# Performance work log

Measured on AMD Instinct MI355X. Metric: run time of the kernel, lower is better.

The kernel has to match this reference:

```python
import jax, jax.numpy as jnp
import numpy as np

D_MODEL = 1024
NUM_HEADS = 16
D_H = D_MODEL // NUM_HEADS
BATCH, SEQ = 4, 2048


def setup_inputs() -> dict:
    key = jax.random.key(0)
    kx, kq, kk, kv, ko = jax.random.split(key, 5)
    sigma = (2.0 / (D_MODEL + D_MODEL)) ** 0.5

    def trunc(k):
        return jax.random.truncated_normal(k, -3.0, 3.0, (D_MODEL, D_MODEL), dtype=jnp.float32) * sigma

    return {
        "x": jax.random.normal(kx, (BATCH, SEQ, D_MODEL), dtype=jnp.float32),
        "Wq": trunc(kq),
        "Wk": trunc(kk),
        "Wv": trunc(kv),
        "Wo": trunc(ko),
    }


def reference(x, Wq, Wk, Wv, Wo):
    B, S, D = x.shape
    H, Dh = NUM_HEADS, D_H
    # Linear: einsum('d_out d_in, ... d_in -> ... d_out')
    q = jnp.einsum('oi,bsi->bso', Wq, x)
    k = jnp.einsum('oi,bsi->bso', Wk, x)
    v = jnp.einsum('oi,bsi->bso', Wv, x)
    # split heads: [B, H, S, Dh]
    q = q.reshape(B, S, H, Dh).transpose(0, 2, 1, 3)
    k = k.reshape(B, S, H, Dh).transpose(0, 2, 1, 3)
    v = v.reshape(B, S, H, Dh).transpose(0, 2, 1, 3)
    scale = 1.0 / jnp.sqrt(jnp.asarray(Dh, dtype=x.dtype))
    score = jnp.einsum('bhnd,bhmd->bhnm', q, k) * scale  # [B,H,S,S]
    causal = jnp.tril(jnp.ones((S, S), dtype=bool))
    score = jnp.where(causal, score, -jnp.inf)
    attn = jax.nn.softmax(score, axis=-1)
    out = jnp.einsum('bhnm,bhmd->bhnd', attn, v)
    out = out.transpose(0, 2, 1, 3).reshape(B, S, D)
    return jnp.einsum('oi,bsi->bso', Wo, out)
```

## Files before the change

kernel.cpp:

```cpp
#include <hip/hip_runtime.h>
#include <hip/hip_bf16.h>

typedef __bf16 bf16x8 __attribute__((ext_vector_type(8)));
typedef __bf16 bf16x4 __attribute__((ext_vector_type(4)));
typedef float f32x4 __attribute__((ext_vector_type(4)));
typedef float f32x16 __attribute__((ext_vector_type(16)));

#define NB 4
#define NS 2048
#define ND 1024
#define NH 16
#define NDH 64
#define NM (NB*NS)

#define MFMA(a,b,c)   __builtin_amdgcn_mfma_f32_16x16x32_bf16((a),(b),(c),0,0,0)
#define MFMA32(a,b,c) __builtin_amdgcn_mfma_f32_32x32x16_bf16((a),(b),(c),0,0,0)

__device__ __forceinline__ void gload16(const void* g, void* l) {
    __builtin_amdgcn_global_load_lds(
        (const __attribute__((address_space(1))) void*)(g),
        (__attribute__((address_space(3))) void*)(l),
        16, 0, 0);
}

__device__ __forceinline__ unsigned cvt_pk_bf16(float lo, float hi) {
    unsigned w;
    asm("v_cvt_pk_bf16_f32 %0, %1, %2" : "=v"(w) : "v"(lo), "v"(hi));
    return w;
}
__device__ __forceinline__ float fmax3(float a, float b, float c) {
    float d;
    asm("v_max3_f32 %0, %1, %2, %3" : "=v"(d) : "v"(a), "v"(b), "v"(c));
    return d;
}
#define PLSWAP(a, b) asm("v_permlane32_swap_b32 %0, %1" : "+v"(a), "+v"(b))

__global__ __launch_bounds__(256) void cast4(const float* __restrict__ in,
                                             __bf16* __restrict__ out, int n) {
    int i = (blockIdx.x * 256 + threadIdx.x) * 4;
    if (i >= n) return;
    float4 v = *(const float4*)(in + i);
    bf16x4 o;
    o[0] = (__bf16)v.x; o[1] = (__bf16)v.y; o[2] = (__bf16)v.z; o[3] = (__bf16)v.w;
    *(bf16x4*)(out + i) = o;
}

__global__ __launch_bounds__(256) void cast4w(
    const float* __restrict__ w0, const float* __restrict__ w1,
    const float* __restrict__ w2, const float* __restrict__ w3,
    __bf16* __restrict__ o0, __bf16* __restrict__ o1,
    __bf16* __restrict__ o2, __bf16* __restrict__ o3) {
    const int z = blockIdx.y;
    const float* in  = (z == 0) ? w0 : (z == 1) ? w1 : (z == 2) ? w2 : w3;
    __bf16*      out = (z == 0) ? o0 : (z == 1) ? o1 : (z == 2) ? o2 : o3;
    int i = (blockIdx.x * 256 + threadIdx.x) * 4;
    float4 v = *(const float4*)(in + i);
    bf16x4 o;
    o[0] = (__bf16)v.x; o[1] = (__bf16)v.y; o[2] = (__bf16)v.z; o[3] = (__bf16)v.w;
    *(bf16x4*)(out + i) = o;
}

template<int MODE>
__global__ __launch_bounds__(256) void gemm128(
    const __bf16* __restrict__ A,
    const __bf16* __restrict__ W0, const __bf16* __restrict__ W1,
    const __bf16* __restrict__ W2,
    __bf16* __restrict__ O0, __bf16* __restrict__ O1, __bf16* __restrict__ O2,
    float* __restrict__ Cf)
{
    __shared__ alignas(16) __bf16 SB[2 * 128 * 32];
    __bf16* As = SB;
    __bf16* Bs = SB + 128 * 32;

    const int tid  = threadIdx.x;
    const int wave = tid >> 6, lane = tid & 63;
    const int l16  = lane & 15, lq = lane >> 4;
    const int bm = blockIdx.x * 128;
    const int bn = blockIdx.y * 128;
    const int z  = (MODE == 0) ? blockIdx.z : 0;
    const __bf16* __restrict__ Bw =
        (MODE == 0) ? ((z == 0) ? W0 : (z == 1) ? W1 : W2) : W0;

    const int wr = (wave >> 1) * 64;
    const int wc = (wave & 1) * 64;

    f32x4 acc[4][4];
    #pragma unroll
    for (int i = 0; i < 4; i++)
        #pragma unroll
        for (int j = 0; j < 4; j++)
            acc[i][j] = (f32x4){0.f, 0.f, 0.f, 0.f};

    const int ch0 = tid, ch1 = tid + 256;
    const int r0 = ch0 >> 2, c0 = (ch0 & 3) * 8;
    const int r1 = ch1 >> 2, c1 = (ch1 & 3) * 8;

    for (int k0 = 0; k0 < ND; k0 += 32) {
        __syncthreads();
        gload16(A  + (size_t)(bm + r0) * ND + k0 + c0, As + ch0 * 8);
        gload16(Bw + (size_t)(bn + r0) * ND + k0 + c0, Bs + ch0 * 8);
        gload16(A  + (size_t)(bm + r1) * ND + k0 + c1, As + ch1 * 8);
        gload16(Bw + (size_t)(bn + r1) * ND + k0 + c1, Bs + ch1 * 8);
        __syncthreads();

        bf16x8 af[4], bf[4];
        #pragma unroll
        for (int i = 0; i < 4; i++) {
            af[i] = *(const bf16x8*)(As + (wr + i*16 + l16) * 32 + lq * 8);
            bf[i] = *(const bf16x8*)(Bs + (wc + i*16 + l16) * 32 + lq * 8);
        }
        #pragma unroll
        for (int i = 0; i < 4; i++)
            #pragma unroll
            for (int j = 0; j < 4; j++)
                acc[i][j] = MFMA(af[i], bf[j], acc[i][j]);
    }

    if (MODE == 0 && z == 2) {
        __bf16* T = SB;
        const int TP = 136;
        #pragma unroll 1
        for (int c = 0; c < 4; ++c) {
            __syncthreads();
            #pragma unroll
            for (int j = 0; j < 4; j++) {
                if (((wc + j * 16) >> 5) != c) continue;
                #pragma unroll
                for (int i = 0; i < 4; i++)
                    #pragma unroll
                    for (int r = 0; r < 4; r++) {
                        int row = wr + i*16 + lq*4 + r;
                        int col = wc + j*16 + l16 - c*32;
                        T[col * TP + row] = (__bf16)acc[i][j][r];
                    }
            }
            __syncthreads();
            #pragma unroll
            for (int u2 = 0; u2 < 2; u2++) {
                int idx  = tid + u2 * 256;
                int trow = idx >> 4, tu = idx & 15;
                int gcol = bn + c*32 + trow;
                int gs   = bm + tu * 8;
                bf16x8 val = *(const bf16x8*)&T[trow * TP + tu * 8];
                int hh = gcol >> 6, dh = gcol & 63;
                *(bf16x8*)&O2[(((size_t)(gs >> 11) * NH + hh) * NDH + dh) * NS
                              + (gs & 2047)] = val;
            }
        }
        return;
    }

    #pragma unroll
    for (int i = 0; i < 4; i++) {
        #pragma unroll
        for (int j = 0; j < 4; j++) {
            #pragma unroll
            for (int r = 0; r < 4; r++) {
                int row = bm + wr + i*16 + lq*4 + r;
                int col = bn + wc + j*16 + l16;
                float v = acc[i][j][r];
                if (MODE == 1) {
                    Cf[(size_t)row * ND + col] = v;
                } else {
                    if (z == 0) v *= 0.1803368801111204f;
                    int b = row >> 11, s = row & 2047;
                    int h = col >> 6,  dh = col & 63;
                    __bf16* dst = (z == 0) ? O0 : O1;
                    dst[(((size_t)b*NH + h)*NS + s)*NDH + dh] = (__bf16)v;
                }
            }
        }
    }
}

__global__ __launch_bounds__(256) void attn_st(
    const __bf16* __restrict__ Q, const __bf16* __restrict__ K,
    const __bf16* __restrict__ Vt, __bf16* __restrict__ Oa)
{
    __shared__ alignas(16) __bf16 Ks[32*64];
    __shared__ alignas(16) __bf16 Vs[64*32];
    __shared__ float Fs[4][32];

    const int tid  = threadIdx.x;
    const int wave = tid >> 6, lane = tid & 63;
    const int qq   = lane & 31, hi = lane >> 5;

    const int bid = blockIdx.x;
    const int jg  = 15 - (bid >> 6);
    const int bh  = (bid & 7) * 8 + ((bid >> 3) & 7);
    const int j   = 4 * jg + wave;
    const int q0  = 32 * j;
    const int nt  = 4 * jg + 4;

    const int b = bh >> 4, h = bh & 15;
    const size_t qkb = (size_t)bh * NS * NDH;
    const size_t vbb = (size_t)bh * NDH * NS;
    float* Fw = Fs[wave];

    bf16x8 qf[4];
    {
        const __bf16* qr = Q + qkb + (size_t)(q0 + qq) * NDH + hi * 8;
        #pragma unroll
        for (int c = 0; c < 4; c++) qf[c] = *(const bf16x8*)(qr + c * 16);
    }

    f32x16 o0 = (f32x16)0.f, o1 = (f32x16)0.f;
    float mr = -__builtin_inff(), lsum = 0.f;

    const int kr = tid >> 3, ku = tid & 7;
    const int vd = tid >> 2, vu = tid & 3;
    const __bf16* ksrc = K  + qkb + (size_t)kr * NDH + (size_t)((ku ^ (kr & 7)) * 8);
    const __bf16* vsrc = Vt + vbb + (size_t)vd * NS  + (size_t)((vu ^ ((vd >> 1) & 3)) * 8);
    __bf16* kdst = Ks + tid * 8;
    __bf16* vdst = Vs + tid * 8;

    const int vsw = (qq >> 1) & 3;

    #pragma unroll 1
    for (int t = 0; t < nt; ++t) {
        __syncthreads();
        gload16(ksrc, kdst);
        gload16(vsrc, vdst);
        asm volatile("s_waitcnt vmcnt(0)" ::: "memory");
        __syncthreads();

        if (t <= j) {
            bf16x8 kf[4], vf[4];
            #pragma unroll
            for (int c = 0; c < 4; c++)
                kf[c] = *(const bf16x8*)(Ks + qq * 64 + ((2 * c + hi) ^ (qq & 7)) * 8);
            vf[0] = *(const bf16x8*)(Vs + qq * 32        + ((hi)     ^ vsw) * 8);
            vf[1] = *(const bf16x8*)(Vs + qq * 32        + ((2 + hi) ^ vsw) * 8);
            vf[2] = *(const bf16x8*)(Vs + (qq + 32) * 32 + ((hi)     ^ vsw) * 8);
            vf[3] = *(const bf16x8*)(Vs + (qq + 32) * 32 + ((2 + hi) ^ vsw) * 8);

            f32x16 s = (f32x16)0.f;
            __builtin_amdgcn_s_setprio(1);
            #pragma unroll
            for (int c = 0; c < 4; c++) s = MFMA32(kf[c], qf[c], s);
            __builtin_amdgcn_s_setprio(0);

            if (t == j) {
                #pragma unroll
                for (int r = 0; r < 16; r++) {
                    const int crow = (r & 3) + 8 * (r >> 2) + 4 * hi;
                    if (crow > qq) s[r] = -__builtin_inff();
                }
            }

            float a0 = fmax3(s[0],  s[1],  s[2]);
            float a1 = fmax3(s[3],  s[4],  s[5]);
            float a2 = fmax3(s[6],  s[7],  s[8]);
            float a3 = fmax3(s[9],  s[10], s[11]);
            float a4 = fmax3(s[12], s[13], s[14]);
            float tm = fmaxf(fmax3(a0, a1, a2), fmax3(a3, a4, s[15]));

            if (__any(tm > mr + 8.f)) {
                float rowm = fmaxf(tm, __shfl_xor(tm, 32));
                float mnew = fmaxf(mr, rowm);
                float fac  = exp2f(mr - mnew);
                mr = mnew; lsum *= fac;
                if (lane < 32) Fw[qq] = fac;
                f32x4 f0 = *(const f32x4*)&Fw[4 * hi];
                f32x4 f1 = *(const f32x4*)&Fw[8 + 4 * hi];
                f32x4 f2 = *(const f32x4*)&Fw[16 + 4 * hi];
                f32x4 f3 = *(const f32x4*)&Fw[24 + 4 * hi];
                #pragma unroll
                for (int i = 0; i < 4; i++) {
                    o0[i]      *= f0[i]; o1[i]      *= f0[i];
                    o0[4 + i]  *= f1[i]; o1[4 + i]  *= f1[i];
                    o0[8 + i]  *= f2[i]; o1[8 + i]  *= f2[i];
                    o0[12 + i] *= f3[i]; o1[12 + i] *= f3[i];
                }
            }

            float pv[16]; float psum = 0.f;
            #pragma unroll
            for (int r = 0; r < 16; r++) { pv[r] = exp2f(s[r] - mr); psum += pv[r]; }
            lsum += psum;

            unsigned w0 = cvt_pk_bf16(pv[0],  pv[1]);
            unsigned w1 = cvt_pk_bf16(pv[2],  pv[3]);
            unsigned w2 = cvt_pk_bf16(pv[4],  pv[5]);
            unsigned w3 = cvt_pk_bf16(pv[6],  pv[7]);
            unsigned w4 = cvt_pk_bf16(pv[8],  pv[9]);
            unsigned w5 = cvt_pk_bf16(pv[10], pv[11]);
            unsigned w6 = cvt_pk_bf16(pv[12], pv[13]);
            unsigned w7 = cvt_pk_bf16(pv[14], pv[15]);
            PLSWAP(w0, w2); PLSWAP(w1, w3);
            PLSWAP(w4, w6); PLSWAP(w5, w7);
            bf16x8 pa0 = __builtin_bit_cast(bf16x8, (uint4){w0, w1, w2, w3});
            bf16x8 pa1 = __builtin_bit_cast(bf16x8, (uint4){w4, w5, w6, w7});

            __builtin_amdgcn_s_setprio(1);
            o0 = MFMA32(pa0, vf[0], o0);
            o0 = MFMA32(pa1, vf[1], o0);
            o1 = MFMA32(pa0, vf[2], o1);
            o1 = MFMA32(pa1, vf[3], o1);
            __builtin_amdgcn_s_setprio(0);
        }

        ksrc += 32 * NDH;
        vsrc += 32;
    }

    lsum += __shfl_xor(lsum, 32);
    if (lane < 32) Fw[qq] = 1.f / lsum;
    f32x4 i0 = *(const f32x4*)&Fw[4 * hi];
    f32x4 i1 = *(const f32x4*)&Fw[8 + 4 * hi];
    f32x4 i2 = *(const f32x4*)&Fw[16 + 4 * hi];
    f32x4 i3 = *(const f32x4*)&Fw[24 + 4 * hi];
    __bf16* ob = Oa + ((size_t)b * NS + q0) * ND + h * 64 + qq;
    #pragma unroll
    for (int g2 = 0; g2 < 4; g2++) {
        f32x4 iv = (g2 == 0) ? i0 : (g2 == 1) ? i1 : (g2 == 2) ? i2 : i3;
        #pragma unroll
        for (int i = 0; i < 4; i++) {
            const int row = 8 * g2 + 4 * hi + i;
            ob[(size_t)row * ND]      = (__bf16)(o0[4 * g2 + i] * iv[i]);
            ob[(size_t)row * ND + 32] = (__bf16)(o1[4 * g2 + i] * iv[i]);
        }
    }
}

extern "C" void kernel_launch(void* const* d_in, const int* in_sizes, int n_in,
                              void* d_out, int out_size, void* d_ws, size_t ws_size,
                              hipStream_t stream) {
    const float* x  = (const float*)d_in[0];
    const float* wq = (const float*)d_in[1];
    const float* wk = (const float*)d_in[2];
    const float* wv = (const float*)d_in[3];
    const float* wo = (const float*)d_in[4];
    char* ws = (char*)d_ws;

    __bf16* xb  = (__bf16*)(ws);
    __bf16* wqb = (__bf16*)(ws + (16ull << 20));
    __bf16* wkb = (__bf16*)(ws + (18ull << 20));
    __bf16* wvb = (__bf16*)(ws + (20ull << 20));
    __bf16* wob = (__bf16*)(ws + (22ull << 20));
    __bf16* Qb  = (__bf16*)(ws + (24ull << 20));
    __bf16* Kb  = (__bf16*)(ws + (40ull << 20));
    __bf16* Vtb = (__bf16*)(ws + (56ull << 20));
    __bf16* Ab  = (__bf16*)(ws + (72ull << 20));
    float* out  = (float*)d_out;

    cast4<<<dim3(NM * ND / 1024), 256, 0, stream>>>(x, xb, NM * ND);
    cast4w<<<dim3(ND * ND / 1024, 4), 256, 0, stream>>>(
        wq, wk, wv, wo, wqb, wkb, wvb, wob);

    gemm128<0><<<dim3(NM/128, ND/128, 3), 256, 0, stream>>>(
        xb, wqb, wkb, wvb, Qb, Kb, Vtb, nullptr);

    attn_st<<<dim3(1024), 256, 0, stream>>>(Qb, Kb, Vtb, Ab);

    gemm128<1><<<dim3(NM/128, ND/128), 256, 0, stream>>>(
        Ab, wob, nullptr, nullptr, nullptr, nullptr, nullptr, out);
}
```

Baseline: 186.9 us.

## Fuse x cast into QKV GEMM, widen GEMM tiles, register-prefetch attention K/V

Drops the separate fp32-to-bf16 cast kernel for x. The QKV GEMM now loads fp32 x directly, converts it in registers and writes it to swizzled LDS, prefetching the next k-slice. The GEMMs move to 128x256 tiles with K=64 steps, 512 threads and an XOR swizzle to cut LDS bank conflicts. The attention kernel replaces direct global-to-LDS loads with register prefetch of the next K/V tile, overlapping the loads with compute. In exchange, register and LDS use go up and the grid gets fewer blocks.

```diff
diff --git a/kernel.cpp b/kernel.cpp
--- a/kernel.cpp
+++ b/kernel.cpp
@@ -34,16 +34,6 @@
     return d;
 }
 #define PLSWAP(a, b) asm("v_permlane32_swap_b32 %0, %1" : "+v"(a), "+v"(b))
-
-__global__ __launch_bounds__(256) void cast4(const float* __restrict__ in,
-                                             __bf16* __restrict__ out, int n) {
-    int i = (blockIdx.x * 256 + threadIdx.x) * 4;
-    if (i >= n) return;
-    float4 v = *(const float4*)(in + i);
-    bf16x4 o;
-    o[0] = (__bf16)v.x; o[1] = (__bf16)v.y; o[2] = (__bf16)v.z; o[3] = (__bf16)v.w;
-    *(bf16x4*)(out + i) = o;
-}
 
 __global__ __launch_bounds__(256) void cast4w(
     const float* __restrict__ w0, const float* __restrict__ w1,
@@ -61,28 +51,27 @@
 }
 
 template<int MODE>
-__global__ __launch_bounds__(256) void gemm128(
-    const __bf16* __restrict__ A,
+__global__ __launch_bounds__(512) void gemmfs(
+    const float* __restrict__ Xf, const __bf16* __restrict__ Abf,
     const __bf16* __restrict__ W0, const __bf16* __restrict__ W1,
     const __bf16* __restrict__ W2,
     __bf16* __restrict__ O0, __bf16* __restrict__ O1, __bf16* __restrict__ O2,
     float* __restrict__ Cf)
 {
-    __shared__ alignas(16) __bf16 SB[2 * 128 * 32];
-    __bf16* As = SB;
-    __bf16* Bs = SB + 128 * 32;
+    __shared__ alignas(16) __bf16 As[128*64];
+    __shared__ alignas(16) __bf16 Bs[256*64];
 
     const int tid  = threadIdx.x;
     const int wave = tid >> 6, lane = tid & 63;
     const int l16  = lane & 15, lq = lane >> 4;
     const int bm = blockIdx.x * 128;
-    const int bn = blockIdx.y * 128;
+    const int bn = blockIdx.y * 256;
     const int z  = (MODE == 0) ? blockIdx.z : 0;
     const __bf16* __restrict__ Bw =
         (MODE == 0) ? ((z == 0) ? W0 : (z == 1) ? W1 : W2) : W0;
 
-    const int wr = (wave >> 1) * 64;
-    const int wc = (wave & 1) * 64;
+    const int wr = (wave >> 2) * 64;
+    const int wc = (wave & 3) * 64;
 
     f32x4 acc[4][4];
     #pragma unroll
@@ -91,36 +80,82 @@
         for (int j = 0; j < 4; j++)
             acc[i][j] = (f32x4){0.f, 0.f, 0.f, 0.f};
 
-    const int ch0 = tid, ch1 = tid + 256;
-    const int r0 = ch0 >> 2, c0 = (ch0 & 3) * 8;
-    const int r1 = ch1 >> 2, c1 = (ch1 & 3) * 8;
-
-    for (int k0 = 0; k0 < ND; k0 += 32) {
+    const int arow = tid >> 3;
+    const int au   = (tid & 7) ^ (arow & 7);
+    const __bf16* Bg0 = Bw + (size_t)(bn + arow) * ND + au * 8;
+    const __bf16* Bg1 = Bg0 + (size_t)64 * ND;
+    const __bf16* Bg2 = Bg0 + (size_t)128 * ND;
+    const __bf16* Bg3 = Bg0 + (size_t)192 * ND;
+    const float* Xa0 = (MODE == 0) ? Xf + (size_t)(bm + arow) * ND + au * 8 : nullptr;
+    const float* Xa1 = (MODE == 0) ? Xa0 + (size_t)64 * ND : nullptr;
+    const __bf16* Ag0 = (MODE == 1) ? Abf + (size_t)(bm + arow) * ND + au * 8 : nullptr;
+    const __bf16* Ag1 = (MODE == 1) ? Ag0 + (size_t)64 * ND : nullptr;
+
+    const int asw = l16 & 7;
+
+    f32x4 ar[4];
+    if (MODE == 0) {
+        ar[0] = *(const f32x4*)(Xa0);
+        ar[1] = *(const f32x4*)(Xa0 + 4);
+        ar[2] = *(const f32x4*)(Xa1);
+        ar[3] = *(const f32x4*)(Xa1 + 4);
+    }
+
+    #pragma unroll 1
+    for (int t = 0; t < 16; ++t) {
+        const int k0 = t * 64;
         __syncthreads();
-        gload16(A  + (size_t)(bm + r0) * ND + k0 + c0, As + ch0 * 8);
-        gload16(Bw + (size_t)(bn + r0) * ND + k0 + c0, Bs + ch0 * 8);
-        gload16(A  + (size_t)(bm + r1) * ND + k0 + c1, As + ch1 * 8);
-        gload16(Bw + (size_t)(bn + r1) * ND + k0 + c1, Bs + ch1 * 8);
+        if (MODE == 0) {
+            uint4 wA0 = {cvt_pk_bf16(ar[0][0], ar[0][1]), cvt_pk_bf16(ar[0][2], ar[0][3]),
+                         cvt_pk_bf16(ar[1][0], ar[1][1]), cvt_pk_bf16(ar[1][2], ar[1][3])};
+            uint4 wA1 = {cvt_pk_bf16(ar[2][0], ar[2][1]), cvt_pk_bf16(ar[2][2], ar[2][3]),
+                         cvt_pk_bf16(ar[3][0], ar[3][1]), cvt_pk_bf16(ar[3][2], ar[3][3])};
+            *(uint4*)(As + tid * 8)         = wA0;
+            *(uint4*)(As + (tid + 512) * 8) = wA1;
+        } else {
+            gload16(Ag0 + k0, As + tid * 8);
+            gload16(Ag1 + k0, As + (tid + 512) * 8);
+        }
+        gload16(Bg0 + k0, Bs + tid * 8);
+        gload16(Bg1 + k0, Bs + (tid + 512) * 8);
+        gload16(Bg2 + k0, Bs + (tid + 1024) * 8);
+        gload16(Bg3 + k0, Bs + (tid + 1536) * 8);
+        asm volatile("s_waitcnt vmcnt(0)" ::: "memory");
         __syncthreads();
 
-        bf16x8 af[4], bf[4];
-        #pragma unroll
-        for (int i = 0; i < 4; i++) {
-            af[i] = *(const bf16x8*)(As + (wr + i*16 + l16) * 32 + lq * 8);
-            bf[i] = *(const bf16x8*)(Bs + (wc + i*16 + l16) * 32 + lq * 8);
-        }
-        #pragma unroll
-        for (int i = 0; i < 4; i++)
+        if (MODE == 0 && t + 1 < 16) {
+            ar[0] = *(const f32x4*)(Xa0 + k0 + 64);
+            ar[1] = *(const f32x4*)(Xa0 + k0 + 68);
+            ar[2] = *(const f32x4*)(Xa1 + k0 + 64);
+            ar[3] = *(const f32x4*)(Xa1 + k0 + 68);
+        }
+
+        #pragma unroll
+        for (int kk = 0; kk < 2; kk++) {
+            bf16x8 af[4], bfr[4];
+            #pragma unroll
+            for (int i = 0; i < 4; i++)
+                af[i] = *(const bf16x8*)(As + (wr + i*16 + l16) * 64
+                                          + ((kk*4 + lq) ^ asw) * 8);
             #pragma unroll
             for (int j = 0; j < 4; j++)
-                acc[i][j] = MFMA(af[i], bf[j], acc[i][j]);
+                bfr[j] = *(const bf16x8*)(Bs + (wc + j*16 + l16) * 64
+                                           + ((kk*4 + lq) ^ asw) * 8);
+            __builtin_amdgcn_s_setprio(1);
+            #pragma unroll
+            for (int i = 0; i < 4; i++)
+                #pragma unroll
+                for (int j = 0; j < 4; j++)
+                    acc[i][j] = MFMA(af[i], bfr[j], acc[i][j]);
+            __builtin_amdgcn_s_setprio(0);
+        }
     }
 
     if (MODE == 0 && z == 2) {
-        __bf16* T = SB;
+        __bf16* T = As;
         const int TP = 136;
         #pragma unroll 1
-        for (int c = 0; c < 4; ++c) {
+        for (int c = 0; c < 8; ++c) {
             __syncthreads();
             #pragma unroll
             for (int j = 0; j < 4; j++) {
@@ -135,10 +170,8 @@
                     }
             }
             __syncthreads();
-            #pragma unroll
-            for (int u2 = 0; u2 < 2; u2++) {
-                int idx  = tid + u2 * 256;
-                int trow = idx >> 4, tu = idx & 15;
+            {
+                int trow = tid >> 4, tu = tid & 15;
                 int gcol = bn + c*32 + trow;
                 int gs   = bm + tu * 8;
                 bf16x8 val = *(const bf16x8*)&T[trow * TP + tu * 8];
@@ -173,7 +206,7 @@
     }
 }
 
-__global__ __launch_bounds__(256) void attn_st(
+__global__ __launch_bounds__(256) void attn_rs(
     const __bf16* __restrict__ Q, const __bf16* __restrict__ K,
     const __bf16* __restrict__ Vt, __bf16* __restrict__ Oa)
 {
@@ -216,13 +249,22 @@
 
     const int vsw = (qq >> 1) & 3;
 
+    bf16x8 kreg = *(const bf16x8*)ksrc;
+    bf16x8 vreg = *(const bf16x8*)vsrc;
+    ksrc += 32 * NDH; vsrc += 32;
+
     #pragma unroll 1
     for (int t = 0; t < nt; ++t) {
         __syncthreads();
-        gload16(ksrc, kdst);
-        gload16(vsrc, vdst);
-        asm volatile("s_waitcnt vmcnt(0)" ::: "memory");
+        *(bf16x8*)kdst = kreg;
+        *(bf16x8*)vdst = vreg;
         __syncthreads();
+
+        if (t + 1 < nt) {
+            kreg = *(const bf16x8*)ksrc;
+            vreg = *(const bf16x8*)vsrc;
+            ksrc += 32 * NDH; vsrc += 32;
+        }
 
         if (t <= j) {
             bf16x8 kf[4], vf[4];
@@ -299,9 +341,6 @@
             o1 = MFMA32(pa1, vf[3], o1);
             __builtin_amdgcn_s_setprio(0);
         }
-
-        ksrc += 32 * NDH;
-        vsrc += 32;
     }
 
     lsum += __shfl_xor(lsum, 32);
@@ -333,7 +372,6 @@
     const float* wo = (const float*)d_in[4];
     char* ws = (char*)d_ws;
 
-    __bf16* xb  = (__bf16*)(ws);
     __bf16* wqb = (__bf16*)(ws + (16ull << 20));
     __bf16* wkb = (__bf16*)(ws + (18ull << 20));
     __bf16* wvb = (__bf16*)(ws + (20ull << 20));
@@ -344,15 +382,14 @@
     __bf16* Ab  = (__bf16*)(ws + (72ull << 20));
     float* out  = (float*)d_out;
 
-    cast4<<<dim3(NM * ND / 1024), 256, 0, stream>>>(x, xb, NM * ND);
     cast4w<<<dim3(ND * ND / 1024, 4), 256, 0, stream>>>(
         wq, wk, wv, wo, wqb, wkb, wvb, wob);
 
-    gemm128<0><<<dim3(NM/128, ND/128, 3), 256, 0, stream>>>(
-        xb, wqb, wkb, wvb, Qb, Kb, Vtb, nullptr);
-
-    attn_st<<<dim3(1024), 256, 0, stream>>>(Qb, Kb, Vtb, Ab);
-
-    gemm128<1><<<dim3(NM/128, ND/128), 256, 0, stream>>>(
-        Ab, wob, nullptr, nullptr, nullptr, nullptr, nullptr, out);
-}
+    gemmfs<0><<<dim3(NM/128, ND/256, 3), 512, 0, stream>>>(
+        x, nullptr, wqb, wkb, wvb, Qb, Kb, Vtb, nullptr);
+
+    attn_rs<<<dim3(1024), 256, 0, stream>>>(Qb, Kb, Vtb, Ab);
+
+    gemmfs<1><<<dim3(NM/128, ND/256), 512, 0, stream>>>(
+        nullptr, Ab, wob, nullptr, nullptr, nullptr, nullptr, nullptr, out);
+}
```

New measurement: 191.3 us. 1.02x slower.
